# Optimization experiments

Hardware: AMD Instinct MI355X
Metric: run time of the kernel (lower is better)

Reference implementation:

```python
import jax, jax.numpy as jnp
import numpy as np

# Clause structure: 4 unary clauses and 4 binary (joined-space) clauses,
# each with 3 literals; first literal negated ('n' prefix).
U_IDX = np.array([[0, 1, 2], [3, 4, 5], [6, 7, 8], [9, 10, 11]], dtype=np.int32)
U_SIGNS = np.array([[-1.0, 1.0, 1.0]] * 4, dtype=np.float32)
# Joined matrix columns: [u[i1] (0..15), u[i2] (16..31), binary (32..35)]
B_IDX = np.array([[0, 16, 32], [1, 17, 33], [2, 18, 34], [3, 19, 35]], dtype=np.int32)
B_SIGNS = np.array([[-1.0, 1.0, 1.0]] * 4, dtype=np.float32)

N_NODES, N_UNARY = 50000, 16
N_EDGES, N_BINARY = 1600000, 4
INIT_W = 0.5


def setup_inputs() -> dict:
    key = jax.random.key(0)
    k1, k2, k3, k4 = jax.random.split(key, 4)
    unary = jax.random.normal(k1, (N_NODES, N_UNARY), dtype=jnp.float32)
    binary = jax.random.normal(k2, (N_EDGES, N_BINARY), dtype=jnp.float32)
    edge_index = jax.random.randint(k3, (2, N_EDGES), 0, N_NODES, dtype=jnp.int32)
    wu = jnp.full((4,), INIT_W, dtype=jnp.float32)  # learnable unary clause weights
    wb = jnp.full((4,), INIT_W, dtype=jnp.float32)  # learnable binary clause weights
    return {"unary": unary, "binary": binary, "wu": wu, "wb": wb, "edge_index": edge_index}


def _knowledge_enhancer(x, idx, signs, w):
    """x: [R, P]; idx/signs: [C, L]; w: [C]. Returns summed deltas [R, P]."""
    lit = x[:, idx] * signs                                    # [R, C, L] signed literals
    d = (w[:, None] * jax.nn.softmax(lit, axis=-1)) * signs    # [R, C, L] signed deltas
    return jnp.zeros_like(x).at[:, idx].add(d)                 # scatter-sum over clauses


def reference(unary, binary, wu, wb, edge_index):
    i1, i2 = edge_index[0], edge_index[1]
    P = unary.shape[1]
    # Unary knowledge enhancement
    u = unary + _knowledge_enhancer(unary, U_IDX, U_SIGNS, wu)
    # Join: per-edge [u[i1] | u[i2] | binary]
    joined = jnp.concatenate([u[i1], u[i2], binary], axis=1)   # [E, 2P+B]
    d = _knowledge_enhancer(joined, B_IDX, B_SIGNS, wb)        # [E, 2P+B]
    # GroupBy: scatter node blocks back, keep binary block
    n = unary.shape[0]
    delta_up = (jax.ops.segment_sum(d[:, :P], i1, num_segments=n)
                + jax.ops.segment_sum(d[:, P:2 * P], i2, num_segments=n))
    delta_bp = d[:, 2 * P:]
    # activation = identity (default)
    return u + delta_up, binary + delta_bp
```

## Files before the change

kernel.cpp:

```cpp
#include <hip/hip_runtime.h>
#include <hip/hip_bf16.h>

#define N_NODES 50000
#define N_UNARY 16
#define N_EDGES 1600000
#define N_BINARY 4

typedef float vfloat4 __attribute__((ext_vector_type(4)));

#define FP_SCALE 127.0f
#define FP_INV   (1.0f / 127.0f)

#define BUCKET_SHIFT 11
#define BUCKET_NODES 2048
#define N_BUCKETS 25
#define N_GROUPS 50
#define SEG_CAP 73728
#define N_CHUNKS 10

#define SCAT_BLOCK 1024
#define SCAT_RECS (2 * SCAT_BLOCK)

#define SEG_BYTES  ((size_t)N_GROUPS * SEG_CAP * 8)
#define PART_BYTES ((size_t)N_GROUPS * N_CHUNKS * BUCKET_NODES * 8)
#define WS_NEEDED  (SEG_BYTES + 256 + PART_BYTES)

__device__ inline void enhance_u4(const float x[6], float wu0, float wu1,
                                  float u[4]) {
    float l0 = -x[0], l1 = x[1], l2 = x[2];
    float m  = fmaxf(l0, fmaxf(l1, l2));
    float e0 = __expf(l0 - m), e1 = __expf(l1 - m), e2 = __expf(l2 - m);
    float inv = 1.0f / (e0 + e1 + e2);
    u[0] = x[0] - wu0 * e0 * inv;
    u[1] = x[1] + wu0 * e1 * inv;
    u[2] = x[2] + wu0 * e2 * inv;
    float l3 = -x[3], l4 = x[4], l5 = x[5];
    float m2 = fmaxf(l3, fmaxf(l4, l5));
    float f0 = __expf(l3 - m2), f1 = __expf(l4 - m2), f2 = __expf(l5 - m2);
    float inv2 = 1.0f / (f0 + f1 + f2);
    u[3] = x[3] - wu1 * f0 * inv2;
}

__device__ inline void edge_math(const float* unary, const float* binary,
                                 float wu0, float wu1, const float wc[4],
                                 int i1, int i2, int e,
                                 float s0[4], float s1[4],
                                 float* out_b) {
    const float4* u1p = (const float4*)(unary + (size_t)i1 * N_UNARY);
    const float4* u2p = (const float4*)(unary + (size_t)i2 * N_UNARY);
    float4 x1a = u1p[0], x1b = u1p[1];
    float4 x2a = u2p[0], x2b = u2p[1];
    float xa[6] = {x1a.x, x1a.y, x1a.z, x1a.w, x1b.x, x1b.y};
    float xb[6] = {x2a.x, x2a.y, x2a.z, x2a.w, x2b.x, x2b.y};
    float a[4], b[4];
    enhance_u4(xa, wu0, wu1, a);
    enhance_u4(xb, wu0, wu1, b);

    vfloat4 bn = __builtin_nontemporal_load((const vfloat4*)binary + e);
    float bb[4] = {bn.x, bn.y, bn.z, bn.w};
    float ob[4];
#pragma unroll
    for (int c = 0; c < 4; ++c) {
        float l0 = -a[c], l1 = b[c], l2 = bb[c];
        float m  = fmaxf(l0, fmaxf(l1, l2));
        float e0 = __expf(l0 - m);
        float e1 = __expf(l1 - m);
        float e2 = __expf(l2 - m);
        float inv = 1.0f / (e0 + e1 + e2);
        s0[c] = e0 * inv;
        s1[c] = e1 * inv;
        ob[c] = bb[c] + wc[c] * e2 * inv;
    }
    vfloat4 obv = {ob[0], ob[1], ob[2], ob[3]};
    __builtin_nontemporal_store(obv, (vfloat4*)out_b + e);
}

__device__ inline unsigned long long make_rec(const float s[4], int local_id,
                                              int g) {
    unsigned v0 = __float2uint_rn(s[0] * FP_SCALE);
    unsigned v1 = __float2uint_rn(s[1] * FP_SCALE);
    unsigned v2 = __float2uint_rn(s[2] * FP_SCALE);
    unsigned v3 = __float2uint_rn(s[3] * FP_SCALE);
    unsigned pl = v0 | (v1 << 7) | (v2 << 14) | (v3 << 21);
    return (unsigned long long)pl |
           ((unsigned long long)(unsigned)local_id << 28) |
           ((unsigned long long)(unsigned)g << 40);
}

__device__ inline unsigned long long pack4_16(const float s[4]) {
    unsigned long long a = __float2uint_rn(s[0] * FP_SCALE);
    unsigned long long b = __float2uint_rn(s[1] * FP_SCALE);
    unsigned long long c = __float2uint_rn(s[2] * FP_SCALE);
    unsigned long long d = __float2uint_rn(s[3] * FP_SCALE);
    return a | (b << 16) | (c << 32) | (d << 48);
}

__global__ void __launch_bounds__(SCAT_BLOCK)
kenn_edge_scatter_kernel(const float* __restrict__ unary,
                         const float* __restrict__ binary,
                         const float* __restrict__ wu,
                         const float* __restrict__ wb,
                         const int* __restrict__ edge_index,
                         unsigned long long* __restrict__ segs,
                         unsigned* __restrict__ tails,
                         float* __restrict__ out_b) {
    __shared__ unsigned l_cnt[N_GROUPS];
    __shared__ unsigned l_pref[N_GROUPS + 1];
    __shared__ unsigned l_gbase[N_GROUPS];
    __shared__ unsigned long long staged[SCAT_RECS];

    int tid = threadIdx.x;
    if (tid < N_GROUPS) l_cnt[tid] = 0;
    __syncthreads();

    int e = blockIdx.x * SCAT_BLOCK + tid;
    bool valid = (e < N_EDGES);

    int g1 = 0, g2 = 0;
    unsigned pos1 = 0, pos2 = 0;
    unsigned long long rec1 = 0, rec2 = 0;

    if (valid) {
        int i1 = __builtin_nontemporal_load(edge_index + e);
        int i2 = __builtin_nontemporal_load(edge_index + N_EDGES + e);
        float wu0 = wu[0], wu1 = wu[1];
        float wc[4] = {wb[0], wb[1], wb[2], wb[3]};
        float s0[4], s1[4];
        edge_math(unary, binary, wu0, wu1, wc, i1, i2, e, s0, s1, out_b);
        g1 = i1 >> BUCKET_SHIFT;
        g2 = N_BUCKETS + (i2 >> BUCKET_SHIFT);
        rec1 = make_rec(s0, i1 & (BUCKET_NODES - 1), g1);
        rec2 = make_rec(s1, i2 & (BUCKET_NODES - 1), g2);
        pos1 = atomicAdd(&l_cnt[g1], 1u);
        pos2 = atomicAdd(&l_cnt[g2], 1u);
    }
    __syncthreads();

    if (tid == 0) {
        unsigned run = 0;
#pragma unroll
        for (int g = 0; g < N_GROUPS; ++g) { l_pref[g] = run; run += l_cnt[g]; }
        l_pref[N_GROUPS] = run;
    } else if (tid >= 64 && tid < 64 + N_GROUPS) {
        int g = tid - 64;
        unsigned c = l_cnt[g];
        l_gbase[g] = c ? atomicAdd(tails + g, c) : 0u;
    }
    __syncthreads();

    if (valid) {
        staged[l_pref[g1] + pos1] = rec1;
        staged[l_pref[g2] + pos2] = rec2;
    }
    __syncthreads();

    unsigned total = l_pref[N_GROUPS];
    for (unsigned i = tid; i < total; i += SCAT_BLOCK) {
        unsigned long long rec = staged[i];
        unsigned g = (unsigned)(rec >> 40) & 63u;
        unsigned p = l_gbase[g] + (i - l_pref[g]);
        if (p < SEG_CAP)
            __builtin_nontemporal_store(rec & 0xFFFFFFFFFFull,
                                        segs + (size_t)g * SEG_CAP + p);
    }
}

__global__ void __launch_bounds__(512)
kenn_reduce_kernel(const unsigned long long* __restrict__ segs,
                   const unsigned* __restrict__ tails,
                   unsigned long long* __restrict__ partials) {
    __shared__ unsigned long long lacc[BUCKET_NODES];
    int chunk = blockIdx.x;
    int g     = blockIdx.y;
    int tid   = threadIdx.x;

    for (int i = tid; i < BUCKET_NODES; i += blockDim.x) lacc[i] = 0ull;
    __syncthreads();

    unsigned cnt = tails[g];
    if (cnt > SEG_CAP) cnt = SEG_CAP;
    unsigned csz   = (cnt + N_CHUNKS - 1) / N_CHUNKS;
    unsigned start = chunk * csz;
    unsigned end   = start + csz;
    if (end > cnt) end = cnt;

    const unsigned long long* seg = segs + (size_t)g * SEG_CAP;
    unsigned i = start + tid;
    for (; i + 512 < end; i += 1024) {
        unsigned long long ra = seg[i];
        unsigned long long rb = seg[i + 512];
        unsigned ida = (unsigned)(ra >> 28) & (BUCKET_NODES - 1);
        unsigned idb = (unsigned)(rb >> 28) & (BUCKET_NODES - 1);
        unsigned pa = (unsigned)ra & 0x0FFFFFFFu;
        unsigned pb = (unsigned)rb & 0x0FFFFFFFu;
        unsigned long long ea =
            (unsigned long long)(pa & 127u) |
            ((unsigned long long)(pa & (127u << 7))  << 9)  |
            ((unsigned long long)(pa & (127u << 14)) << 18) |
            ((unsigned long long)(pa & (127u << 21)) << 27);
        unsigned long long eb =
            (unsigned long long)(pb & 127u) |
            ((unsigned long long)(pb & (127u << 7))  << 9)  |
            ((unsigned long long)(pb & (127u << 14)) << 18) |
            ((unsigned long long)(pb & (127u << 21)) << 27);
        atomicAdd(&lacc[ida], ea);
        atomicAdd(&lacc[idb], eb);
    }
    for (; i < end; i += 512) {
        unsigned long long r = seg[i];
        unsigned id = (unsigned)(r >> 28) & (BUCKET_NODES - 1);
        unsigned pl = (unsigned)r & 0x0FFFFFFFu;
        unsigned long long exp =
            (unsigned long long)(pl & 127u) |
            ((unsigned long long)(pl & (127u << 7))  << 9)  |
            ((unsigned long long)(pl & (127u << 14)) << 18) |
            ((unsigned long long)(pl & (127u << 21)) << 27);
        atomicAdd(&lacc[id], exp);
    }
    __syncthreads();

    unsigned long long* dst =
        partials + ((size_t)g * N_CHUNKS + chunk) * BUCKET_NODES;
    for (int k = tid; k < BUCKET_NODES; k += blockDim.x)
        __builtin_nontemporal_store(lacc[k], dst + k);
}

__global__ void kenn_node_final_kernel(const float* __restrict__ unary,
                                       const float* __restrict__ wu,
                                       const float* __restrict__ wb,
                                       const unsigned long long* __restrict__ partials,
                                       const unsigned long long* __restrict__ accN,
                                       const unsigned long long* __restrict__ accP,
                                       int use_partials,
                                       float* __restrict__ out_u) {
    int node = blockIdx.x * blockDim.x + threadIdx.x;
    if (node >= N_NODES) return;

    const float4* up = (const float4*)(unary + (size_t)node * N_UNARY);
    float4 x0 = up[0], x1 = up[1], x2 = up[2], x3 = up[3];
    float x[16] = {x0.x, x0.y, x0.z, x0.w,
                   x1.x, x1.y, x1.z, x1.w,
                   x2.x, x2.y, x2.z, x2.w,
                   x3.x, x3.y, x3.z, x3.w};
    float wuc[4] = {wu[0], wu[1], wu[2], wu[3]};

    float y[16];
#pragma unroll
    for (int i = 0; i < 16; ++i) y[i] = x[i];

#pragma unroll
    for (int c = 0; c < 4; ++c) {
        float l0 = -x[3 * c + 0];
        float l1 =  x[3 * c + 1];
        float l2 =  x[3 * c + 2];
        float m  = fmaxf(l0, fmaxf(l1, l2));
        float e0 = __expf(l0 - m);
        float e1 = __expf(l1 - m);
        float e2 = __expf(l2 - m);
        float inv = 1.0f / (e0 + e1 + e2);
        y[3 * c + 0] -= wuc[c] * e0 * inv;
        y[3 * c + 1] += wuc[c] * e1 * inv;
        y[3 * c + 2] += wuc[c] * e2 * inv;
    }

    unsigned long long pn, pp;
    if (use_partials) {
        int bucket = node >> BUCKET_SHIFT;
        int local  = node & (BUCKET_NODES - 1);
        const unsigned long long* pN =
            partials + ((size_t)bucket * N_CHUNKS) * BUCKET_NODES + local;
        const unsigned long long* pP =
            partials + ((size_t)(N_BUCKETS + bucket) * N_CHUNKS) * BUCKET_NODES + local;
        pn = 0ull; pp = 0ull;
#pragma unroll
        for (int c = 0; c < N_CHUNKS; ++c) {
            pn += pN[(size_t)c * BUCKET_NODES];
            pp += pP[(size_t)c * BUCKET_NODES];
        }
    } else {
        pn = accN[node];
        pp = accP[node];
    }

    float wbc[4] = {wb[0], wb[1], wb[2], wb[3]};
    y[0] += wbc[0] * ((float)(int)((pp      ) & 0xffff) - (float)(int)((pn      ) & 0xffff)) * FP_INV;
    y[1] += wbc[1] * ((float)(int)((pp >> 16) & 0xffff) - (float)(int)((pn >> 16) & 0xffff)) * FP_INV;
    y[2] += wbc[2] * ((float)(int)((pp >> 32) & 0xffff) - (float)(int)((pn >> 32) & 0xffff)) * FP_INV;
    y[3] += wbc[3] * ((float)(int)((pp >> 48) & 0xffff) - (float)(int)((pn >> 48) & 0xffff)) * FP_INV;

    float4* op = (float4*)(out_u + (size_t)node * N_UNARY);
    op[0] = make_float4(y[0],  y[1],  y[2],  y[3]);
    op[1] = make_float4(y[4],  y[5],  y[6],  y[7]);
    op[2] = make_float4(y[8],  y[9],  y[10], y[11]);
    op[3] = make_float4(y[12], y[13], y[14], y[15]);
}

__global__ void kenn_edge_atomic_kernel(const float* __restrict__ unary,
                                        const float* __restrict__ binary,
                                        const float* __restrict__ wu,
                                        const float* __restrict__ wb,
                                        const int* __restrict__ edge_index,
                                        unsigned long long* __restrict__ accN,
                                        unsigned long long* __restrict__ accP,
                                        float* __restrict__ out_b) {
    int e = blockIdx.x * blockDim.x + threadIdx.x;
    if (e >= N_EDGES) return;
    int i1 = __builtin_nontemporal_load(edge_index + e);
    int i2 = __builtin_nontemporal_load(edge_index + N_EDGES + e);
    float wu0 = wu[0], wu1 = wu[1];
    float wc[4] = {wb[0], wb[1], wb[2], wb[3]};
    float s0[4], s1[4];
    edge_math(unary, binary, wu0, wu1, wc, i1, i2, e, s0, s1, out_b);
    atomicAdd(accN + i1, pack4_16(s0));
    atomicAdd(accP + i2, pack4_16(s1));
}

extern "C" void kernel_launch(void* const* d_in, const int* in_sizes, int n_in,
                              void* d_out, int out_size, void* d_ws, size_t ws_size,
                              hipStream_t stream) {
    const float* unary      = (const float*)d_in[0];
    const float* binary     = (const float*)d_in[1];
    const float* wu         = (const float*)d_in[2];
    const float* wb         = (const float*)d_in[3];
    const int*   edge_index = (const int*)d_in[4];

    float* out_u = (float*)d_out;
    float* out_b = (float*)d_out + (size_t)N_NODES * N_UNARY;

    if (ws_size >= WS_NEEDED) {
        unsigned long long* segs = (unsigned long long*)d_ws;
        unsigned* tails = (unsigned*)((char*)d_ws + SEG_BYTES);
        unsigned long long* partials =
            (unsigned long long*)((char*)d_ws + SEG_BYTES + 256);

        (void)hipMemsetAsync(tails, 0, N_GROUPS * sizeof(unsigned), stream);
        {
            dim3 grid((N_EDGES + SCAT_BLOCK - 1) / SCAT_BLOCK);
            kenn_edge_scatter_kernel<<<grid, dim3(SCAT_BLOCK), 0, stream>>>(
                unary, binary, wu, wb, edge_index, segs, tails, out_b);
        }
        {
            dim3 grid(N_CHUNKS, N_GROUPS);
            kenn_reduce_kernel<<<grid, dim3(512), 0, stream>>>(
                segs, tails, partials);
        }
        {
            dim3 block(256);
            dim3 grid((N_NODES + 255) / 256);
            kenn_node_final_kernel<<<grid, block, 0, stream>>>(
                unary, wu, wb, partials, nullptr, nullptr, 1, out_u);
        }
    } else {
        unsigned long long* accN = (unsigned long long*)d_ws;
        unsigned long long* accP = accN + N_NODES;
        (void)hipMemsetAsync(accN, 0,
                             (size_t)N_NODES * 2 * sizeof(unsigned long long),
                             stream);
        {
            dim3 block(256);
            dim3 grid((N_EDGES + 255) / 256);
            kenn_edge_atomic_kernel<<<grid, block, 0, stream>>>(
                unary, binary, wu, wb, edge_index, accN, accP, out_b);
        }
        {
            dim3 block(256);
            dim3 grid((N_NODES + 255) / 256);
            kenn_node_final_kernel<<<grid, block, 0, stream>>>(
                unary, wu, wb, nullptr, accN, accP, 0, out_u);
        }
    }
}
```

Before: 151.5 us.

## Precompute enhanced unary literals per node and gather compact float4 per edge

Adds a per-node kernel that computes the four unary-enhanced literals needed by the binary clauses and stores them as a float4 array in workspace. The edge scatter kernel then gathers 16 bytes per endpoint instead of 32 bytes of raw unary, and no longer recomputes two softmaxes per endpoint for every edge. It also moves the shared-memory bucket counting ahead of the gathers and replaces the serial prefix sum with a wavefront shuffle scan. This costs one extra small kernel launch and a larger workspace requirement, which could push execution onto the atomic fallback path if the workspace is too small.

```diff
diff --git a/kernel.cpp b/kernel.cpp
--- a/kernel.cpp
+++ b/kernel.cpp
@@ -23,7 +23,8 @@
 
 #define SEG_BYTES  ((size_t)N_GROUPS * SEG_CAP * 8)
 #define PART_BYTES ((size_t)N_GROUPS * N_CHUNKS * BUCKET_NODES * 8)
-#define WS_NEEDED  (SEG_BYTES + 256 + PART_BYTES)
+#define U4_BYTES   ((size_t)N_NODES * 16)
+#define WS_NEEDED  (SEG_BYTES + 256 + PART_BYTES + U4_BYTES)
 
 __device__ inline void enhance_u4(const float x[6], float wu0, float wu1,
                                   float u[4]) {
@@ -41,22 +42,12 @@
     u[3] = x[3] - wu1 * f0 * inv2;
 }
 
-__device__ inline void edge_math(const float* unary, const float* binary,
-                                 float wu0, float wu1, const float wc[4],
-                                 int i1, int i2, int e,
-                                 float s0[4], float s1[4],
-                                 float* out_b) {
-    const float4* u1p = (const float4*)(unary + (size_t)i1 * N_UNARY);
-    const float4* u2p = (const float4*)(unary + (size_t)i2 * N_UNARY);
-    float4 x1a = u1p[0], x1b = u1p[1];
-    float4 x2a = u2p[0], x2b = u2p[1];
-    float xa[6] = {x1a.x, x1a.y, x1a.z, x1a.w, x1b.x, x1b.y};
-    float xb[6] = {x2a.x, x2a.y, x2a.z, x2a.w, x2b.x, x2b.y};
-    float a[4], b[4];
-    enhance_u4(xa, wu0, wu1, a);
-    enhance_u4(xb, wu0, wu1, b);
-
-    vfloat4 bn = __builtin_nontemporal_load((const vfloat4*)binary + e);
+__device__ inline void clause_math(float4 a4, float4 b4, vfloat4 bn,
+                                   const float wc[4], int e,
+                                   float s0[4], float s1[4],
+                                   float* out_b) {
+    float a[4]  = {a4.x, a4.y, a4.z, a4.w};
+    float b[4]  = {b4.x, b4.y, b4.z, b4.w};
     float bb[4] = {bn.x, bn.y, bn.z, bn.w};
     float ob[4];
 #pragma unroll
@@ -95,10 +86,22 @@
     return a | (b << 16) | (c << 32) | (d << 48);
 }
 
+__global__ void kenn_u4_kernel(const float* __restrict__ unary,
+                               const float* __restrict__ wu,
+                               float* __restrict__ u4) {
+    int node = blockIdx.x * blockDim.x + threadIdx.x;
+    if (node >= N_NODES) return;
+    const float4* up = (const float4*)(unary + (size_t)node * N_UNARY);
+    float4 xa = up[0], xb = up[1];
+    float x[6] = {xa.x, xa.y, xa.z, xa.w, xb.x, xb.y};
+    float u[4];
+    enhance_u4(x, wu[0], wu[1], u);
+    ((float4*)u4)[node] = make_float4(u[0], u[1], u[2], u[3]);
+}
+
 __global__ void __launch_bounds__(SCAT_BLOCK)
-kenn_edge_scatter_kernel(const float* __restrict__ unary,
+kenn_edge_scatter_kernel(const float* __restrict__ u4,
                          const float* __restrict__ binary,
-                         const float* __restrict__ wu,
                          const float* __restrict__ wb,
                          const int* __restrict__ edge_index,
                          unsigned long long* __restrict__ segs,
@@ -123,24 +126,32 @@
     if (valid) {
         int i1 = __builtin_nontemporal_load(edge_index + e);
         int i2 = __builtin_nontemporal_load(edge_index + N_EDGES + e);
-        float wu0 = wu[0], wu1 = wu[1];
+        g1 = i1 >> BUCKET_SHIFT;
+        g2 = N_BUCKETS + (i2 >> BUCKET_SHIFT);
+        pos1 = atomicAdd(&l_cnt[g1], 1u);
+        pos2 = atomicAdd(&l_cnt[g2], 1u);
+
+        float4 a4 = ((const float4*)u4)[i1];
+        float4 b4 = ((const float4*)u4)[i2];
+        vfloat4 bn = __builtin_nontemporal_load((const vfloat4*)binary + e);
         float wc[4] = {wb[0], wb[1], wb[2], wb[3]};
         float s0[4], s1[4];
-        edge_math(unary, binary, wu0, wu1, wc, i1, i2, e, s0, s1, out_b);
-        g1 = i1 >> BUCKET_SHIFT;
-        g2 = N_BUCKETS + (i2 >> BUCKET_SHIFT);
+        clause_math(a4, b4, bn, wc, e, s0, s1, out_b);
         rec1 = make_rec(s0, i1 & (BUCKET_NODES - 1), g1);
         rec2 = make_rec(s1, i2 & (BUCKET_NODES - 1), g2);
-        pos1 = atomicAdd(&l_cnt[g1], 1u);
-        pos2 = atomicAdd(&l_cnt[g2], 1u);
-    }
-    __syncthreads();
-
-    if (tid == 0) {
-        unsigned run = 0;
+    }
+    __syncthreads();
+
+    if (tid < 64) {
+        unsigned v = (tid < N_GROUPS) ? l_cnt[tid] : 0u;
+        unsigned s = v;
 #pragma unroll
-        for (int g = 0; g < N_GROUPS; ++g) { l_pref[g] = run; run += l_cnt[g]; }
-        l_pref[N_GROUPS] = run;
+        for (int off = 1; off < 64; off <<= 1) {
+            unsigned t = __shfl_up(s, off, 64);
+            if (tid >= off) s += t;
+        }
+        if (tid < N_GROUPS) l_pref[tid] = s - v;
+        if (tid == N_GROUPS - 1) l_pref[N_GROUPS] = s;
     } else if (tid >= 64 && tid < 64 + N_GROUPS) {
         int g = tid - 64;
         unsigned c = l_cnt[g];
@@ -309,8 +320,20 @@
     int i2 = __builtin_nontemporal_load(edge_index + N_EDGES + e);
     float wu0 = wu[0], wu1 = wu[1];
     float wc[4] = {wb[0], wb[1], wb[2], wb[3]};
+
+    const float4* u1p = (const float4*)(unary + (size_t)i1 * N_UNARY);
+    const float4* u2p = (const float4*)(unary + (size_t)i2 * N_UNARY);
+    float4 x1a = u1p[0], x1b = u1p[1];
+    float4 x2a = u2p[0], x2b = u2p[1];
+    float xa[6] = {x1a.x, x1a.y, x1a.z, x1a.w, x1b.x, x1b.y};
+    float xb[6] = {x2a.x, x2a.y, x2a.z, x2a.w, x2b.x, x2b.y};
+    float a[4], b[4];
+    enhance_u4(xa, wu0, wu1, a);
+    enhance_u4(xb, wu0, wu1, b);
+    vfloat4 bn = __builtin_nontemporal_load((const vfloat4*)binary + e);
     float s0[4], s1[4];
-    edge_math(unary, binary, wu0, wu1, wc, i1, i2, e, s0, s1, out_b);
+    clause_math(make_float4(a[0], a[1], a[2], a[3]),
+                make_float4(b[0], b[1], b[2], b[3]), bn, wc, e, s0, s1, out_b);
     atomicAdd(accN + i1, pack4_16(s0));
     atomicAdd(accP + i2, pack4_16(s1));
 }
@@ -332,12 +355,18 @@
         unsigned* tails = (unsigned*)((char*)d_ws + SEG_BYTES);
         unsigned long long* partials =
             (unsigned long long*)((char*)d_ws + SEG_BYTES + 256);
+        float* u4 = (float*)((char*)d_ws + SEG_BYTES + 256 + PART_BYTES);
 
         (void)hipMemsetAsync(tails, 0, N_GROUPS * sizeof(unsigned), stream);
+        {
+            dim3 block(256);
+            dim3 grid((N_NODES + 255) / 256);
+            kenn_u4_kernel<<<grid, block, 0, stream>>>(unary, wu, u4);
+        }
         {
             dim3 grid((N_EDGES + SCAT_BLOCK - 1) / SCAT_BLOCK);
             kenn_edge_scatter_kernel<<<grid, dim3(SCAT_BLOCK), 0, stream>>>(
-                unary, binary, wu, wb, edge_index, segs, tails, out_b);
+                u4, binary, wb, edge_index, segs, tails, out_b);
         }
         {
             dim3 grid(N_CHUNKS, N_GROUPS);
```

Result: no change. 152.2 us (+0.5%).
